# Kernel optimization log

Hardware: AMD Instinct MI355X
Metric: run time of the kernel (lower is better)

## Reference

```python
import jax, jax.numpy as jnp
import numpy as np

HIDDEN = 2048
NUM_EXPERTS = 64
TOP_K = 2


def setup_inputs() -> dict:
    key = jax.random.key(0)
    k1, k2 = jax.random.split(key)
    x = jax.random.normal(k1, (4, 4096, HIDDEN), dtype=jnp.float32)
    # nn.Linear(hidden, num_experts, bias=False): weight shape [E, H], y = x @ W.T
    W = jax.random.normal(k2, (NUM_EXPERTS, HIDDEN), dtype=jnp.float32) * (HIDDEN ** -0.5)
    return {"x": x, "W": W}


def reference(x, W):
    B, S, H = x.shape
    E, K = NUM_EXPERTS, TOP_K
    xf = x.reshape(-1, H)                       # [N, H]
    gate_logits = xf @ W.T                      # [N, E]
    routing_probs = jax.nn.softmax(gate_logits, axis=-1)
    top_k_probs, top_k_indices = jax.lax.top_k(routing_probs, K)  # [N, K]
    denom = jnp.sum(top_k_probs, axis=-1, keepdims=True) + 1e-6
    routing_weights = (top_k_probs / denom).reshape(B, S, K)
    expert_indices = top_k_indices.reshape(B, S, K)

    # aux load-balancing loss (training path)
    N = xf.shape[0]
    # expert_mask.mean(0): fraction of tokens assigned to each expert
    assign_per_expert = jnp.zeros((E,), jnp.float32).at[top_k_indices.reshape(-1)].add(1.0) / N
    prob_per_expert = jnp.mean(routing_probs, axis=0)             # [E]
    aux_loss = (jnp.sum(prob_per_expert * prob_per_expert) * E
                + jnp.sum(assign_per_expert * assign_per_expert) * E)

    # expert_counts update (bincount over selected indices)
    expert_counts = jnp.zeros((E,), jnp.float32).at[top_k_indices.reshape(-1)].add(1.0)

    return routing_weights, expert_indices, aux_loss, expert_counts
```

## Files before the change

### kernel.cpp

```cpp
#include <hip/hip_runtime.h>

#define HID 2048
#define NEXP 64
#define NTOK 16384
#define TM 32
#define NTHREADS 256
#define NCHUNK 32
#define RS 72
#define PLANE_S 4608
#define PLANE_B 9216
#define CHUNK_B 27648
#define WS_W_OFF 1024

#define OUT_IDX_OFF (2 * NTOK)
#define OUT_AUX_OFF (4 * NTOK)
#define OUT_CNT_OFF (4 * NTOK + 1)

typedef __attribute__((ext_vector_type(8))) short bhalf8;
typedef __attribute__((ext_vector_type(4))) float f32x4;

__device__ __forceinline__ void split3(float v, unsigned short& h1, unsigned short& h2, unsigned short& h3) {
    unsigned int u = __float_as_uint(v);
    unsigned int r1 = (u + 0x7FFFu + ((u >> 16) & 1u)) & 0xFFFF0000u;
    float f1 = __uint_as_float(r1);
    float d1 = v - f1;
    unsigned int u2 = __float_as_uint(d1);
    unsigned int r2 = (u2 + 0x7FFFu + ((u2 >> 16) & 1u)) & 0xFFFF0000u;
    float f2 = __uint_as_float(r2);
    float d2 = d1 - f2;
    h1 = (unsigned short)(r1 >> 16);
    h2 = (unsigned short)(r2 >> 16);
    h3 = (unsigned short)(__float_as_uint(d2) >> 16);
}

__device__ __forceinline__ void make_frags(float4 va, float4 vb, bhalf8& o1, bhalf8& o2, bhalf8& o3) {
    float f[8] = {va.x, va.y, va.z, va.w, vb.x, vb.y, vb.z, vb.w};
    union U { bhalf8 v; unsigned int u[4]; } u1, u2, u3;
#pragma unroll
    for (int t = 0; t < 4; t++) {
        unsigned short a1, a2, a3, b1, b2, b3;
        split3(f[2 * t], a1, a2, a3);
        split3(f[2 * t + 1], b1, b2, b3);
        u1.u[t] = (unsigned int)a1 | ((unsigned int)b1 << 16);
        u2.u[t] = (unsigned int)a2 | ((unsigned int)b2 << 16);
        u3.u[t] = (unsigned int)a3 | ((unsigned int)b3 << 16);
    }
    o1 = u1.v; o2 = u2.v; o3 = u3.v;
}

__global__ __launch_bounds__(256) void wsplit_kernel(const float* __restrict__ W,
                                                     char* __restrict__ wq,
                                                     float* __restrict__ wsf) {
    if (blockIdx.x == 0 && threadIdx.x < 2 * NEXP) wsf[threadIdx.x] = 0.f;
    int idx8 = (blockIdx.x * 256 + threadIdx.x) * 8;
    int e = idx8 >> 11;
    int kk = idx8 & 2047;
    int c = kk >> 6;
    int j = kk & 63;
    const float4* wp = (const float4*)(W + (size_t)e * HID + kk);
    float4 v0 = wp[0], v1 = wp[1];
    float f[8] = {v0.x, v0.y, v0.z, v0.w, v1.x, v1.y, v1.z, v1.w};
    unsigned int p1[4], p2[4], p3[4];
#pragma unroll
    for (int t = 0; t < 4; t++) {
        unsigned short a1, a2, a3, b1, b2, b3;
        split3(f[2 * t], a1, a2, a3);
        split3(f[2 * t + 1], b1, b2, b3);
        p1[t] = (unsigned int)a1 | ((unsigned int)b1 << 16);
        p2[t] = (unsigned int)a2 | ((unsigned int)b2 << 16);
        p3[t] = (unsigned int)a3 | ((unsigned int)b3 << 16);
    }
    char* base = wq + (size_t)c * CHUNK_B + e * (RS * 2) + j * 2;
    *(uint4*)(base)               = make_uint4(p1[0], p1[1], p1[2], p1[3]);
    *(uint4*)(base + PLANE_B)     = make_uint4(p2[0], p2[1], p2[2], p2[3]);
    *(uint4*)(base + 2 * PLANE_B) = make_uint4(p3[0], p3[1], p3[2], p3[3]);
}

__device__ __forceinline__ void dma_w_chunk(const char* gbase, char* lbase, int wave, int lane) {
#pragma unroll
    for (int k = 0; k < 7; k++) {
        int idx = wave + 4 * k;
        if (idx < 27) {
            __builtin_amdgcn_global_load_lds(
                (const __attribute__((address_space(1))) unsigned int*)(gbase + idx * 1024 + lane * 16),
                (__attribute__((address_space(3))) unsigned int*)(lbase + idx * 1024 + lane * 16),
                16, 0, 0);
        }
    }
}

__global__ __launch_bounds__(NTHREADS, 2) void router_main(
    const float* __restrict__ x, const char* __restrict__ wq,
    float* __restrict__ out, float* __restrict__ ws_accum)
{
    __shared__ __align__(16) char wpl[2 * CHUNK_B];
    __shared__ float smax[TM];
    __shared__ float sinvZ[TM];
    __shared__ float scount[NEXP];

    const int tid = threadIdx.x;
    const int wave = tid >> 6;
    const int lane = tid & 63;
    const int m = lane & 15;
    const int q = lane >> 4;
    const int tokhalf = wave & 1;
    const int exphalf = wave >> 1;
    const int n0 = blockIdx.x * TM;

    const float* xrow = x + (size_t)(n0 + tokhalf * 16 + m) * HID + q * 8;

    f32x4 acc[2][2] = {{{0.f,0.f,0.f,0.f},{0.f,0.f,0.f,0.f}},
                       {{0.f,0.f,0.f,0.f},{0.f,0.f,0.f,0.f}}};

    dma_w_chunk(wq, wpl, wave, lane);
    float4 px[2][2];
    px[0][0] = *(const float4*)(xrow);
    px[0][1] = *(const float4*)(xrow + 4);
    px[1][0] = *(const float4*)(xrow + 32);
    px[1][1] = *(const float4*)(xrow + 36);

#pragma unroll 1
    for (int c = 0; c < NCHUNK; ++c) {
        __syncthreads();
        if (c + 1 < NCHUNK)
            dma_w_chunk(wq + (size_t)(c + 1) * CHUNK_B, wpl + ((c + 1) & 1) * CHUNK_B, wave, lane);

        bhalf8 A[2][3];
        make_frags(px[0][0], px[0][1], A[0][0], A[0][1], A[0][2]);
        make_frags(px[1][0], px[1][1], A[1][0], A[1][1], A[1][2]);

        if (c + 1 < NCHUNK) {
            const float* xp = xrow + (c + 1) * 64;
            px[0][0] = *(const float4*)(xp);
            px[0][1] = *(const float4*)(xp + 4);
            px[1][0] = *(const float4*)(xp + 32);
            px[1][1] = *(const float4*)(xp + 36);
        }

        const unsigned short* wb = (const unsigned short*)(wpl + (c & 1) * CHUNK_B);
#pragma unroll
        for (int kc = 0; kc < 2; ++kc) {
#pragma unroll
            for (int t = 0; t < 2; ++t) {
                const int bo = (exphalf * 32 + t * 16 + m) * RS + kc * 32 + q * 8;
                bhalf8 b1 = *(const bhalf8*)(wb + 0 * PLANE_S + bo);
                bhalf8 b2 = *(const bhalf8*)(wb + 1 * PLANE_S + bo);
                bhalf8 b3 = *(const bhalf8*)(wb + 2 * PLANE_S + bo);
                f32x4 a4 = acc[t][kc];
                a4 = __builtin_amdgcn_mfma_f32_16x16x32_bf16(A[kc][0], b1, a4, 0, 0, 0);
                a4 = __builtin_amdgcn_mfma_f32_16x16x32_bf16(A[kc][0], b2, a4, 0, 0, 0);
                a4 = __builtin_amdgcn_mfma_f32_16x16x32_bf16(A[kc][1], b1, a4, 0, 0, 0);
                a4 = __builtin_amdgcn_mfma_f32_16x16x32_bf16(A[kc][0], b3, a4, 0, 0, 0);
                a4 = __builtin_amdgcn_mfma_f32_16x16x32_bf16(A[kc][1], b2, a4, 0, 0, 0);
                a4 = __builtin_amdgcn_mfma_f32_16x16x32_bf16(A[kc][2], b1, a4, 0, 0, 0);
                a4 = __builtin_amdgcn_mfma_f32_16x16x32_bf16(A[kc][1], b3, a4, 0, 0, 0);
                a4 = __builtin_amdgcn_mfma_f32_16x16x32_bf16(A[kc][2], b2, a4, 0, 0, 0);
                a4 = __builtin_amdgcn_mfma_f32_16x16x32_bf16(A[kc][2], b3, a4, 0, 0, 0);
                acc[t][kc] = a4;
            }
        }
    }

    float* logits = (float*)wpl;
    {
        const int col = lane & 15;
        const int rbase = (lane >> 4) * 4;
#pragma unroll
        for (int t = 0; t < 2; ++t)
#pragma unroll
            for (int r = 0; r < 4; ++r)
                logits[(tokhalf * 16 + rbase + r) * 68 + exphalf * 32 + t * 16 + col] =
                    acc[t][0][r] + acc[t][1][r];
    }
    if (tid < NEXP) scount[tid] = 0.f;
    __syncthreads();

    if (tid < TM) {
        const int t = tid;
        float m1 = -3.4e38f, m2 = -3.4e38f;
        int i1 = 0, i2 = 0;
        for (int e = 0; e < NEXP; e++) {
            float v = logits[t * 68 + e];
            if (v > m1) { m2 = m1; i2 = i1; m1 = v; i1 = e; }
            else if (v > m2) { m2 = v; i2 = e; }
        }
        float Z = 0.f;
        for (int e = 0; e < NEXP; e++)
            Z += __expf(logits[t * 68 + e] - m1);
        float invZ = 1.f / Z;
        float p1 = invZ;
        float p2 = __expf(m2 - m1) * invZ;
        float denom = p1 + p2 + 1e-6f;
        int n = n0 + t;
        out[2 * n + 0] = p1 / denom;
        out[2 * n + 1] = p2 / denom;
        out[OUT_IDX_OFF + 2 * n + 0] = (float)i1;
        out[OUT_IDX_OFF + 2 * n + 1] = (float)i2;
        smax[t] = m1;
        sinvZ[t] = invZ;
        atomicAdd(&scount[i1], 1.f);
        atomicAdd(&scount[i2], 1.f);
    }
    __syncthreads();

    if (tid < NEXP) {
        const int e = tid;
        float s = 0.f;
        for (int t = 0; t < TM; t++)
            s += __expf(logits[t * 68 + e] - smax[t]) * sinvZ[t];
        atomicAdd(&ws_accum[e], s);
        atomicAdd(&ws_accum[NEXP + e], scount[e]);
    }
}

__global__ void router_finish(const float* __restrict__ ws_accum,
                              float* __restrict__ out)
{
    const int e = threadIdx.x;
    const float invN = 1.f / (float)NTOK;
    float p = ws_accum[e] * invN;
    float a = ws_accum[NEXP + e] * invN;
    float v = p * p + a * a;
#pragma unroll
    for (int off = 32; off > 0; off >>= 1)
        v += __shfl_down(v, off);
    if (e == 0) out[OUT_AUX_OFF] = v * (float)NEXP;
    out[OUT_CNT_OFF + e] = ws_accum[NEXP + e];
}

extern "C" void kernel_launch(void* const* d_in, const int* in_sizes, int n_in,
                              void* d_out, int out_size, void* d_ws, size_t ws_size,
                              hipStream_t stream)
{
    const float* x = (const float*)d_in[0];
    const float* W = (const float*)d_in[1];
    float* out = (float*)d_out;
    float* wsf = (float*)d_ws;
    char* wq = (char*)d_ws + WS_W_OFF;

    wsplit_kernel<<<64, 256, 0, stream>>>(W, wq, wsf);
    router_main<<<NTOK / TM, NTHREADS, 0, stream>>>(x, wq, out, wsf);
    router_finish<<<1, 64, 0, stream>>>(wsf, out);
}
```

Baseline: 236.2 us.

## Split K across waves with 32x32 MFMA and direct global W fragment loads

Each wave now owns a quarter of the K range for all 32 tokens and all 64 experts, using 32x32x16 bf16 MFMAs. It loads pre-swizzled W fragments straight from global memory instead of double-buffering W chunks through LDS with per-chunk barriers. The three-way bf16 split product drops the three lowest-order cross terms, going from 9 to 6 MFMAs per step, and x is split by truncation rather than rounding. Partial logits are reduced across waves through LDS. This cuts barrier, LDS traffic and MFMA count, but accepts slightly lower precision and more L2 traffic for W.

```diff
diff --git a/kernel.cpp b/kernel.cpp
--- a/kernel.cpp
+++ b/kernel.cpp
@@ -6,18 +6,17 @@
 #define TM 32
 #define NTHREADS 256
 #define NCHUNK 32
-#define RS 72
-#define PLANE_S 4608
-#define PLANE_B 9216
-#define CHUNK_B 27648
+#define KPH 4
+#define CPW 8
 #define WS_W_OFF 1024
+#define CHUNK_B 24576
 
 #define OUT_IDX_OFF (2 * NTOK)
 #define OUT_AUX_OFF (4 * NTOK)
 #define OUT_CNT_OFF (4 * NTOK + 1)
 
 typedef __attribute__((ext_vector_type(8))) short bhalf8;
-typedef __attribute__((ext_vector_type(4))) float f32x4;
+typedef __attribute__((ext_vector_type(16))) float f32x16;
 
 __device__ __forceinline__ void split3(float v, unsigned short& h1, unsigned short& h2, unsigned short& h3) {
     unsigned int u = __float_as_uint(v);
@@ -33,17 +32,21 @@
     h3 = (unsigned short)(__float_as_uint(d2) >> 16);
 }
 
-__device__ __forceinline__ void make_frags(float4 va, float4 vb, bhalf8& o1, bhalf8& o2, bhalf8& o3) {
+__device__ __forceinline__ void xsplit(float4 va, float4 vb, bhalf8& o1, bhalf8& o2, bhalf8& o3) {
     float f[8] = {va.x, va.y, va.z, va.w, vb.x, vb.y, vb.z, vb.w};
     union U { bhalf8 v; unsigned int u[4]; } u1, u2, u3;
 #pragma unroll
     for (int t = 0; t < 4; t++) {
-        unsigned short a1, a2, a3, b1, b2, b3;
-        split3(f[2 * t], a1, a2, a3);
-        split3(f[2 * t + 1], b1, b2, b3);
-        u1.u[t] = (unsigned int)a1 | ((unsigned int)b1 << 16);
-        u2.u[t] = (unsigned int)a2 | ((unsigned int)b2 << 16);
-        u3.u[t] = (unsigned int)a3 | ((unsigned int)b3 << 16);
+        float a = f[2 * t], b = f[2 * t + 1];
+        unsigned int ua = __float_as_uint(a), ub = __float_as_uint(b);
+        float da = a - __uint_as_float(ua & 0xFFFF0000u);
+        float db = b - __uint_as_float(ub & 0xFFFF0000u);
+        unsigned int uda = __float_as_uint(da), udb = __float_as_uint(db);
+        float da2 = da - __uint_as_float(uda & 0xFFFF0000u);
+        float db2 = db - __uint_as_float(udb & 0xFFFF0000u);
+        u1.u[t] = (ua >> 16) | (ub & 0xFFFF0000u);
+        u2.u[t] = (uda >> 16) | (udb & 0xFFFF0000u);
+        u3.u[t] = (__float_as_uint(da2) >> 16) | (__float_as_uint(db2) & 0xFFFF0000u);
     }
     o1 = u1.v; o2 = u2.v; o3 = u3.v;
 }
@@ -54,10 +57,10 @@
     if (blockIdx.x == 0 && threadIdx.x < 2 * NEXP) wsf[threadIdx.x] = 0.f;
     int idx8 = (blockIdx.x * 256 + threadIdx.x) * 8;
     int e = idx8 >> 11;
-    int kk = idx8 & 2047;
-    int c = kk >> 6;
-    int j = kk & 63;
-    const float4* wp = (const float4*)(W + (size_t)e * HID + kk);
+    int k0 = idx8 & 2047;
+    int c = k0 >> 6, ks = (k0 >> 4) & 3, half = (k0 >> 3) & 1;
+    int g = e >> 5, l = (e & 31) + 32 * half;
+    const float4* wp = (const float4*)(W + (size_t)e * HID + k0);
     float4 v0 = wp[0], v1 = wp[1];
     float f[8] = {v0.x, v0.y, v0.z, v0.w, v1.x, v1.y, v1.z, v1.w};
     unsigned int p1[4], p2[4], p3[4];
@@ -70,109 +73,92 @@
         p2[t] = (unsigned int)a2 | ((unsigned int)b2 << 16);
         p3[t] = (unsigned int)a3 | ((unsigned int)b3 << 16);
     }
-    char* base = wq + (size_t)c * CHUNK_B + e * (RS * 2) + j * 2;
-    *(uint4*)(base)               = make_uint4(p1[0], p1[1], p1[2], p1[3]);
-    *(uint4*)(base + PLANE_B)     = make_uint4(p2[0], p2[1], p2[2], p2[3]);
-    *(uint4*)(base + 2 * PLANE_B) = make_uint4(p3[0], p3[1], p3[2], p3[3]);
-}
-
-__device__ __forceinline__ void dma_w_chunk(const char* gbase, char* lbase, int wave, int lane) {
-#pragma unroll
-    for (int k = 0; k < 7; k++) {
-        int idx = wave + 4 * k;
-        if (idx < 27) {
-            __builtin_amdgcn_global_load_lds(
-                (const __attribute__((address_space(1))) unsigned int*)(gbase + idx * 1024 + lane * 16),
-                (__attribute__((address_space(3))) unsigned int*)(lbase + idx * 1024 + lane * 16),
-                16, 0, 0);
-        }
-    }
+    char* base = wq + (size_t)(((c * 4 + ks) * 3 + 0) * 2 + g) * 1024 + l * 16;
+    *(uint4*)(base)        = make_uint4(p1[0], p1[1], p1[2], p1[3]);
+    *(uint4*)(base + 2048) = make_uint4(p2[0], p2[1], p2[2], p2[3]);
+    *(uint4*)(base + 4096) = make_uint4(p3[0], p3[1], p3[2], p3[3]);
 }
 
 __global__ __launch_bounds__(NTHREADS, 2) void router_main(
     const float* __restrict__ x, const char* __restrict__ wq,
     float* __restrict__ out, float* __restrict__ ws_accum)
 {
-    __shared__ __align__(16) char wpl[2 * CHUNK_B];
+    __shared__ float slab[KPH * TM * 68];
     __shared__ float smax[TM];
     __shared__ float sinvZ[TM];
     __shared__ float scount[NEXP];
 
     const int tid = threadIdx.x;
-    const int wave = tid >> 6;
+    const int w = tid >> 6;
     const int lane = tid & 63;
-    const int m = lane & 15;
-    const int q = lane >> 4;
-    const int tokhalf = wave & 1;
-    const int exphalf = wave >> 1;
+    const int r = lane & 31;
+    const int h = lane >> 5;
     const int n0 = blockIdx.x * TM;
 
-    const float* xrow = x + (size_t)(n0 + tokhalf * 16 + m) * HID + q * 8;
-
-    f32x4 acc[2][2] = {{{0.f,0.f,0.f,0.f},{0.f,0.f,0.f,0.f}},
-                       {{0.f,0.f,0.f,0.f},{0.f,0.f,0.f,0.f}}};
-
-    dma_w_chunk(wq, wpl, wave, lane);
-    float4 px[2][2];
-    px[0][0] = *(const float4*)(xrow);
-    px[0][1] = *(const float4*)(xrow + 4);
-    px[1][0] = *(const float4*)(xrow + 32);
-    px[1][1] = *(const float4*)(xrow + 36);
+    const float* xrow = x + (size_t)(n0 + r) * HID + h * 8;
+
+    f32x16 acc0, acc1;
+#pragma unroll
+    for (int i = 0; i < 16; i++) { acc0[i] = 0.f; acc1[i] = 0.f; }
 
 #pragma unroll 1
-    for (int c = 0; c < NCHUNK; ++c) {
-        __syncthreads();
-        if (c + 1 < NCHUNK)
-            dma_w_chunk(wq + (size_t)(c + 1) * CHUNK_B, wpl + ((c + 1) & 1) * CHUNK_B, wave, lane);
-
-        bhalf8 A[2][3];
-        make_frags(px[0][0], px[0][1], A[0][0], A[0][1], A[0][2]);
-        make_frags(px[1][0], px[1][1], A[1][0], A[1][1], A[1][2]);
-
-        if (c + 1 < NCHUNK) {
-            const float* xp = xrow + (c + 1) * 64;
-            px[0][0] = *(const float4*)(xp);
-            px[0][1] = *(const float4*)(xp + 4);
-            px[1][0] = *(const float4*)(xp + 32);
-            px[1][1] = *(const float4*)(xp + 36);
+    for (int i = 0; i < CPW; ++i) {
+        const int c = w * CPW + i;
+        const float* xc = xrow + c * 64;
+        float4 pxa[4], pxb[4];
+#pragma unroll
+        for (int ks = 0; ks < 4; ks++) {
+            pxa[ks] = *(const float4*)(xc + ks * 16);
+            pxb[ks] = *(const float4*)(xc + ks * 16 + 4);
         }
-
-        const unsigned short* wb = (const unsigned short*)(wpl + (c & 1) * CHUNK_B);
-#pragma unroll
-        for (int kc = 0; kc < 2; ++kc) {
-#pragma unroll
-            for (int t = 0; t < 2; ++t) {
-                const int bo = (exphalf * 32 + t * 16 + m) * RS + kc * 32 + q * 8;
-                bhalf8 b1 = *(const bhalf8*)(wb + 0 * PLANE_S + bo);
-                bhalf8 b2 = *(const bhalf8*)(wb + 1 * PLANE_S + bo);
-                bhalf8 b3 = *(const bhalf8*)(wb + 2 * PLANE_S + bo);
-                f32x4 a4 = acc[t][kc];
-                a4 = __builtin_amdgcn_mfma_f32_16x16x32_bf16(A[kc][0], b1, a4, 0, 0, 0);
-                a4 = __builtin_amdgcn_mfma_f32_16x16x32_bf16(A[kc][0], b2, a4, 0, 0, 0);
-                a4 = __builtin_amdgcn_mfma_f32_16x16x32_bf16(A[kc][1], b1, a4, 0, 0, 0);
-                a4 = __builtin_amdgcn_mfma_f32_16x16x32_bf16(A[kc][0], b3, a4, 0, 0, 0);
-                a4 = __builtin_amdgcn_mfma_f32_16x16x32_bf16(A[kc][1], b2, a4, 0, 0, 0);
-                a4 = __builtin_amdgcn_mfma_f32_16x16x32_bf16(A[kc][2], b1, a4, 0, 0, 0);
-                a4 = __builtin_amdgcn_mfma_f32_16x16x32_bf16(A[kc][1], b3, a4, 0, 0, 0);
-                a4 = __builtin_amdgcn_mfma_f32_16x16x32_bf16(A[kc][2], b2, a4, 0, 0, 0);
-                a4 = __builtin_amdgcn_mfma_f32_16x16x32_bf16(A[kc][2], b3, a4, 0, 0, 0);
-                acc[t][kc] = a4;
+        const char* wc = wq + (size_t)c * CHUNK_B + lane * 16;
+#pragma unroll
+        for (int ks = 0; ks < 4; ks++) {
+            bhalf8 A1, A2, A3;
+            xsplit(pxa[ks], pxb[ks], A1, A2, A3);
+            const char* wk = wc + ks * 6144;
+            {
+                bhalf8 B1 = *(const bhalf8*)(wk);
+                bhalf8 B2 = *(const bhalf8*)(wk + 2048);
+                bhalf8 B3 = *(const bhalf8*)(wk + 4096);
+                acc0 = __builtin_amdgcn_mfma_f32_32x32x16_bf16(A1, B1, acc0, 0, 0, 0);
+                acc0 = __builtin_amdgcn_mfma_f32_32x32x16_bf16(A1, B2, acc0, 0, 0, 0);
+                acc0 = __builtin_amdgcn_mfma_f32_32x32x16_bf16(A2, B1, acc0, 0, 0, 0);
+                acc0 = __builtin_amdgcn_mfma_f32_32x32x16_bf16(A1, B3, acc0, 0, 0, 0);
+                acc0 = __builtin_amdgcn_mfma_f32_32x32x16_bf16(A2, B2, acc0, 0, 0, 0);
+                acc0 = __builtin_amdgcn_mfma_f32_32x32x16_bf16(A3, B1, acc0, 0, 0, 0);
+            }
+            {
+                bhalf8 B1 = *(const bhalf8*)(wk + 1024);
+                bhalf8 B2 = *(const bhalf8*)(wk + 2048 + 1024);
+                bhalf8 B3 = *(const bhalf8*)(wk + 4096 + 1024);
+                acc1 = __builtin_amdgcn_mfma_f32_32x32x16_bf16(A1, B1, acc1, 0, 0, 0);
+                acc1 = __builtin_amdgcn_mfma_f32_32x32x16_bf16(A1, B2, acc1, 0, 0, 0);
+                acc1 = __builtin_amdgcn_mfma_f32_32x32x16_bf16(A2, B1, acc1, 0, 0, 0);
+                acc1 = __builtin_amdgcn_mfma_f32_32x32x16_bf16(A1, B3, acc1, 0, 0, 0);
+                acc1 = __builtin_amdgcn_mfma_f32_32x32x16_bf16(A2, B2, acc1, 0, 0, 0);
+                acc1 = __builtin_amdgcn_mfma_f32_32x32x16_bf16(A3, B1, acc1, 0, 0, 0);
             }
         }
     }
 
-    float* logits = (float*)wpl;
-    {
-        const int col = lane & 15;
-        const int rbase = (lane >> 4) * 4;
-#pragma unroll
-        for (int t = 0; t < 2; ++t)
-#pragma unroll
-            for (int r = 0; r < 4; ++r)
-                logits[(tokhalf * 16 + rbase + r) * 68 + exphalf * 32 + t * 16 + col] =
-                    acc[t][0][r] + acc[t][1][r];
+#pragma unroll
+    for (int reg = 0; reg < 16; reg++) {
+        int row = (reg & 3) + 8 * (reg >> 2) + 4 * h;
+        slab[(w * TM + row) * 68 + r]      = acc0[reg];
+        slab[(w * TM + row) * 68 + 32 + r] = acc1[reg];
     }
     if (tid < NEXP) scount[tid] = 0.f;
+    __syncthreads();
+
+    float* logits = slab;
+#pragma unroll
+    for (int idx = tid; idx < TM * NEXP; idx += NTHREADS) {
+        int t = idx >> 6, e = idx & 63;
+        float v = slab[(0 * TM + t) * 68 + e] + slab[(1 * TM + t) * 68 + e]
+                + slab[(2 * TM + t) * 68 + e] + slab[(3 * TM + t) * 68 + e];
+        logits[t * 68 + e] = v;
+    }
     __syncthreads();
 
     if (tid < TM) {
```

After: 217.5 us. 7.9% less time.
